# Kernel optimization log

Hardware: AMD Instinct MI355X
Metric: run time of the kernel (lower is better)

Reference implementation:

```python
import jax, jax.numpy as jnp
import numpy as np

N_NODES = 100000
N_EDGES = 1600000
N_GRAPHS = 256
EPS = 1e-5  # GraphNorm / BatchNorm eps


def _seg_sum(x, seg, n):
    return jax.ops.segment_sum(x, seg, num_segments=n)


def setup_inputs() -> dict:
    key = jax.random.key(0)
    ks = jax.random.split(key, 24)
    f32 = jnp.float32

    def nrm(k, shape, s=0.05):
        return jax.random.normal(k, shape, f32) * s

    inp = {}
    inp["x"] = jax.random.normal(ks[0], (N_NODES, 64), f32)
    inp["edge_attr"] = jax.random.normal(ks[1], (N_EDGES, 8), f32)
    # edge_mlp: Linear(8,16) -> ReLU -> Linear(16,1); final bias +2 keeps degrees positive
    inp["em_w1"] = nrm(ks[2], (16, 8), 0.1); inp["em_b1"] = jnp.zeros((16,), f32)
    inp["em_w2"] = nrm(ks[3], (1, 16), 0.1); inp["em_b2"] = jnp.full((1,), 2.0, f32)
    # GCNConv weights stored (in, out); PyG GCNConv lin has no bias, separate bias after aggregation
    inp["conv_w0"] = nrm(ks[4], (64, 128)); inp["conv_b0"] = jnp.zeros((128,), f32)
    inp["conv_w1"] = nrm(ks[5], (128, 128)); inp["conv_b1"] = jnp.zeros((128,), f32)
    inp["conv_w2"] = nrm(ks[6], (128, 128)); inp["conv_b2"] = jnp.zeros((128,), f32)
    # GraphNorm params: weight=1, bias=0, mean_scale=1 (PyG init)
    for i in range(3):
        inp[f"gn_w{i}"] = jnp.ones((128,), f32)
        inp[f"gn_b{i}"] = jnp.zeros((128,), f32)
        inp[f"gn_ms{i}"] = jnp.ones((128,), f32)
    # MLP head (weights stored (in,out)); BatchNorm1d eval: running_mean=0, running_var=1
    inp["lin_w0"] = nrm(ks[7], (128, 256)); inp["lin_b0"] = jnp.zeros((256,), f32)
    inp["bn_g0"] = jnp.ones((256,), f32); inp["bn_b0"] = jnp.zeros((256,), f32)
    inp["lin_w1"] = nrm(ks[8], (256, 128)); inp["lin_b1"] = jnp.zeros((128,), f32)
    inp["bn_g1"] = jnp.ones((128,), f32); inp["bn_b1"] = jnp.zeros((128,), f32)
    inp["out_w"] = nrm(ks[9], (128, 1)); inp["out_b"] = jnp.zeros((1,), f32)
    inp["edge_index"] = jax.random.randint(ks[10], (2, N_EDGES), 0, N_NODES)
    inp["batch"] = jnp.sort(jax.random.randint(ks[11], (N_NODES,), 0, N_GRAPHS))
    return inp


def _gcn_conv(h, W, b, src, tgt, ew):
    # PyG GCNConv with edge_weight: add self-loops (weight 1), symmetric normalization
    hw = h @ W  # [N, out]
    deg = _seg_sum(ew, tgt, N_NODES) + 1.0  # in-degree incl. self-loop
    dinv = jnp.where(deg > 0, jax.lax.rsqrt(deg), 0.0)
    norm_e = dinv[src] * ew * dinv[tgt]  # [E]
    agg = _seg_sum(norm_e[:, None] * hw[src], tgt, N_NODES)
    agg = agg + (dinv * dinv)[:, None] * hw  # self-loop contribution
    return agg + b


def _graph_norm(h, batch, w, b, ms, cnt):
    mean = _seg_sum(h, batch, N_GRAPHS) / cnt[:, None]  # [G, C]
    sub = h - ms * mean[batch]
    var = _seg_sum(sub * sub, batch, N_GRAPHS) / cnt[:, None]
    return w * sub / jnp.sqrt(var + EPS)[batch] + b


def reference(x, edge_attr, em_w1, em_b1, em_w2, em_b2,
              conv_w0, conv_b0, conv_w1, conv_b1, conv_w2, conv_b2,
              gn_w0, gn_b0, gn_ms0, gn_w1, gn_b1, gn_ms1, gn_w2, gn_b2, gn_ms2,
              lin_w0, lin_b0, bn_g0, bn_b0, lin_w1, lin_b1, bn_g1, bn_b1,
              out_w, out_b, edge_index, batch):
    src, tgt = edge_index[0], edge_index[1]
    ew = (jax.nn.relu(edge_attr @ em_w1.T + em_b1) @ em_w2.T + em_b2).reshape(-1)  # [E]
    cnt = jnp.maximum(_seg_sum(jnp.ones((N_NODES,), x.dtype), batch, N_GRAPHS), 1.0)

    h = x
    layers = [(conv_w0, conv_b0, gn_w0, gn_b0, gn_ms0),
              (conv_w1, conv_b1, gn_w1, gn_b1, gn_ms1),
              (conv_w2, conv_b2, gn_w2, gn_b2, gn_ms2)]
    for W, b, gw, gb, gms in layers:
        h = _gcn_conv(h, W, b, src, tgt, ew)
        h = _graph_norm(h, batch, gw, gb, gms, cnt)
        h = jax.nn.relu(h)  # dropout is identity in eval mode

    pooled = _seg_sum(h, batch, N_GRAPHS) / cnt[:, None]  # global_mean_pool [G, 128]

    inv = 1.0 / jnp.sqrt(1.0 + EPS)  # BatchNorm1d eval: mean=0, var=1
    h = jax.nn.relu((pooled @ lin_w0 + lin_b0) * inv * bn_g0 + bn_b0)
    h = jax.nn.relu((h @ lin_w1 + lin_b1) * inv * bn_g1 + bn_b1)
    out = h @ out_w + out_b  # [G, 1]
    return (out, h)
```

## Files before the change

kernel.cpp:

```cpp
#include <hip/hip_runtime.h>

#define N_NODES 100000
#define N_EDGES 1600000
#define N_GRAPHS 256
#define EPS 1e-5f

#define NBUCK 1024
#define NUSED 782
#define NBLK 256
#define EPB (N_EDGES / NBLK)

#define WB 128
#define W0B 32
#define SB 2
#define PREP_BLOCKS (WB + W0B + SB + NBLK)

typedef __attribute__((ext_vector_type(8))) short bfrag8;
typedef __attribute__((ext_vector_type(4))) float facc4;

__device__ __forceinline__ void fma4(float4& a, float s, const float4& w) {
  a.x += s * w.x; a.y += s * w.y; a.z += s * w.z; a.w += s * w.w;
}

__device__ __forceinline__ unsigned short f2bf(float f) {
  union { float f; unsigned u; } x;
  x.f = f;
  unsigned r = x.u + 0x7FFF + ((x.u >> 16) & 1);
  return (unsigned short)(r >> 16);
}
__device__ __forceinline__ unsigned packbf(float a, float b) {
  return (unsigned)f2bf(a) | ((unsigned)f2bf(b) << 16);
}
__device__ __forceinline__ float4 bf4(unsigned lo, unsigned hi) {
  union { unsigned u; float f; } a, b, c, d;
  a.u = lo << 16;
  b.u = lo & 0xFFFF0000u;
  c.u = hi << 16;
  d.u = hi & 0xFFFF0000u;
  return make_float4(a.f, b.f, c.f, d.f);
}
__device__ __forceinline__ float bfat(const unsigned* tb, int idx) {
  unsigned u = tb[idx >> 1];
  union { unsigned u; float f; } v;
  v.u = (idx & 1) ? (u & 0xFFFF0000u) : (u << 16);
  return v.f;
}

__global__ __launch_bounds__(256) void k_prep(
    const float* __restrict__ cw1, const float* __restrict__ cw2,
    unsigned short* __restrict__ wt1, unsigned short* __restrict__ wt2,
    const float* __restrict__ cw0, unsigned short* __restrict__ wt0,
    const int* __restrict__ batch, int* __restrict__ start,
    const int* __restrict__ tgt, int* __restrict__ hists,
    int* __restrict__ bcnt) {
  __shared__ int h[NBUCK];
  const int b = blockIdx.x;
  const int t = threadIdx.x;
  if (b < WB) {
    int half = b >> 6;
    int id = (b & 63) * 256 + t;
    const float* w = half ? cw2 : cw1;
    unsigned short* o = half ? wt2 : wt1;
    int n = id >> 7, k = id & 127;
    o[n * 128 + k] = f2bf(w[k * 128 + n]);
  } else if (b < WB + W0B) {
    int id = (b - WB) * 256 + t;
    if (id >= 8192) return;
    int n = id >> 6, k = id & 63;
    wt0[n * 64 + k] = f2bf(cw0[k * 128 + n]);
  } else if (b < WB + W0B + SB) {
    int g = (b - WB - W0B) * 256 + t;
    if (g > N_GRAPHS) return;
    int lo = 0, hi = N_NODES;
    while (lo < hi) {
      int mid = (lo + hi) >> 1;
      if (batch[mid] < g) lo = mid + 1; else hi = mid;
    }
    start[g] = lo;
  } else {
    const int blk = b - WB - W0B - SB;
    for (int i = t; i < NBUCK; i += 256) h[i] = 0;
    __syncthreads();
    const int s = blk * EPB, e = s + EPB;
    for (int j = s + t; j < e; j += 256) atomicAdd(&h[tgt[j] >> 7], 1);
    __syncthreads();
    for (int i = t; i < NBUCK; i += 256) {
      int v = h[i];
      hists[blk * NBUCK + i] = v;
      if (v) atomicAdd(&bcnt[i], v);
    }
  }
}

__global__ __launch_bounds__(1024) void k_bscan(const int* __restrict__ bcnt,
                                                int* __restrict__ bbase) {
  __shared__ int s[NBUCK];
  const int b = threadIdx.x;
  int v = bcnt[b];
  s[b] = v;
  __syncthreads();
  for (int off = 1; off < NBUCK; off <<= 1) {
    int u = (b >= off) ? s[b - off] : 0;
    __syncthreads();
    s[b] += u;
    __syncthreads();
  }
  bbase[b] = s[b] - v;
  if (b == NBUCK - 1) bbase[NBUCK] = N_EDGES;
}

__global__ __launch_bounds__(NBLK) void k_cursors(const int* __restrict__ hists,
                                                  const int* __restrict__ bbase,
                                                  int* __restrict__ cursor) {
  __shared__ int s[NBLK];
  const int b = blockIdx.x;
  const int k = threadIdx.x;
  int v = hists[k * NBUCK + b];
  s[k] = v;
  __syncthreads();
  for (int off = 1; off < NBLK; off <<= 1) {
    int u = (k >= off) ? s[k - off] : 0;
    __syncthreads();
    s[k] += u;
    __syncthreads();
  }
  cursor[b * NBLK + k] = bbase[b] + s[k] - v;
}

__global__ __launch_bounds__(256) void k_scatter(
    const float* __restrict__ ea, const float* __restrict__ w1,
    const float* __restrict__ b1, const float* __restrict__ w2,
    const float* __restrict__ b2, const int* __restrict__ src,
    const int* __restrict__ tgt, const int* __restrict__ cursor,
    uint2* __restrict__ mb) {
  __shared__ float W1[128], B1[16], W2[16];
  __shared__ int cur[NBUCK];
  const int blk = blockIdx.x, t = threadIdx.x;
  if (t < 128) W1[t] = w1[t];
  if (t < 16) { B1[t] = b1[t]; W2[t] = w2[t]; }
  for (int i = t; i < NUSED; i += 256) cur[i] = cursor[i * NBLK + blk];
  __syncthreads();
  const int s = blk * EPB, e = s + EPB;
  for (int j = s + t; j < e; j += 256) {
    const float4* ap = (const float4*)(ea + (size_t)j * 8);
    float4 a0 = ap[0], a1 = ap[1];
    float a[8] = {a0.x, a0.y, a0.z, a0.w, a1.x, a1.y, a1.z, a1.w};
    float out = b2[0];
#pragma unroll
    for (int i = 0; i < 16; ++i) {
      float h = B1[i];
#pragma unroll
      for (int jj = 0; jj < 8; ++jj) h += a[jj] * W1[i * 8 + jj];
      out += fmaxf(h, 0.f) * W2[i];
    }
    int d = tgt[j];
    int bin = d >> 7;
    int pos = atomicAdd(&cur[bin], 1);
    union { float f; unsigned u; } w;
    w.f = out;
    mb[pos] = make_uint2(w.u, (unsigned)src[j] | ((unsigned)(d & 127) << 25));
  }
}

__global__ __launch_bounds__(256) void k_csr(
    const uint2* __restrict__ mb, const int* __restrict__ bbase,
    const float* __restrict__ x, uint2* __restrict__ meta,
    int* __restrict__ rowstart, float* __restrict__ dinv,
    unsigned* __restrict__ xb) {
  __shared__ int hist[128];
  __shared__ float degf[128];
  __shared__ int cur[128];
  __shared__ float dls[128];
  const int b = blockIdx.x;
  const int t = threadIdx.x;
  const int s = bbase[b], e = bbase[b + 1];
  if (t < 128) { hist[t] = 0; degf[t] = 0.f; }
  __syncthreads();
  for (int j = s + t; j < e; j += 256) {
    uint2 m = mb[j];
    int bin = m.y >> 25;
    atomicAdd(&hist[bin], 1);
    union { unsigned u; float f; } w;
    w.u = m.x;
    atomicAdd(&degf[bin], w.f);
  }
  __syncthreads();
  int own = (t < 128) ? hist[t] : 0;
  for (int off = 1; off < 128; off <<= 1) {
    int u = (t >= off && t < 128) ? hist[t - off] : 0;
    __syncthreads();
    if (t < 128) hist[t] += u;
    __syncthreads();
  }
  if (t < 128) {
    int excl = hist[t] - own;
    int node = b * 128 + t;
    if (node <= N_NODES) rowstart[node] = s + excl;
    float dv = 0.f;
    if (node < N_NODES) {
      float d = 1.f + degf[t];
      dv = d > 0.f ? rsqrtf(d) : 0.f;
      dinv[node] = dv;
    }
    dls[t] = dv;
    cur[t] = s + excl;
  }
  __syncthreads();
  for (int j = s + t; j < e; j += 256) {
    uint2 m = mb[j];
    int bin = m.y >> 25;
    int pos = atomicAdd(&cur[bin], 1);
    meta[pos] = make_uint2(m.x, m.y & 0x1FFFFFFu);
  }
  {
    const int ln = t >> 1, half = t & 1;
    const int node = b * 128 + ln;
    if (node < N_NODES) {
      float dv = dls[ln];
      const float* px = x + (size_t)node * 64 + half * 32;
#pragma unroll
      for (int c8 = 0; c8 < 4; ++c8) {
        float4 a = *(const float4*)(px + c8 * 8);
        float4 bb = *(const float4*)(px + c8 * 8 + 4);
        uint4 o;
        o.x = packbf(dv * a.x, dv * a.y);
        o.y = packbf(dv * a.z, dv * a.w);
        o.z = packbf(dv * bb.x, dv * bb.y);
        o.w = packbf(dv * bb.z, dv * bb.w);
        *(uint4*)&xb[(size_t)node * 32 + half * 16 + c8 * 4] = o;
      }
    }
  }
}

__global__ __launch_bounds__(256) void k_gather64b(
    const unsigned* __restrict__ xb, const uint2* __restrict__ meta,
    const int* __restrict__ rowstart, const float* __restrict__ dinv,
    unsigned* __restrict__ aggxb) {
  const int t = threadIdx.x;
  const int n = blockIdx.x * 4 + (t >> 6);
  if (n >= N_NODES) return;
  const unsigned lane = t & 63;
  const unsigned q = lane >> 3;
  const unsigned cl = lane & 7;
  const int rs = rowstart[n], re = rowstart[n + 1];
  const uint4* x4 = (const uint4*)xb;
  float4 lo0 = make_float4(0.f, 0.f, 0.f, 0.f), hi0 = lo0;
  float4 lo1 = lo0, hi1 = lo0;
  int j = rs;
  for (; j + 16 <= re; j += 16) {
    uint2 m0 = meta[j + q], m1 = meta[j + 8 + q];
    union { unsigned u; float f; } w0, w1;
    w0.u = m0.x; w1.u = m1.x;
    uint4 v0 = x4[(m0.y << 3) + cl];
    uint4 v1 = x4[(m1.y << 3) + cl];
    fma4(lo0, w0.f, bf4(v0.x, v0.y));
    fma4(hi0, w0.f, bf4(v0.z, v0.w));
    fma4(lo1, w1.f, bf4(v1.x, v1.y));
    fma4(hi1, w1.f, bf4(v1.z, v1.w));
  }
  for (; j + 8 <= re; j += 8) {
    uint2 m0 = meta[j + q];
    union { unsigned u; float f; } w0;
    w0.u = m0.x;
    uint4 v0 = x4[(m0.y << 3) + cl];
    fma4(lo0, w0.f, bf4(v0.x, v0.y));
    fma4(hi0, w0.f, bf4(v0.z, v0.w));
  }
  if (j + (int)q < re) {
    uint2 m0 = meta[j + q];
    union { unsigned u; float f; } w0;
    w0.u = m0.x;
    uint4 v0 = x4[(m0.y << 3) + cl];
    fma4(lo1, w0.f, bf4(v0.x, v0.y));
    fma4(hi1, w0.f, bf4(v0.z, v0.w));
  }
  lo0.x += lo1.x; lo0.y += lo1.y; lo0.z += lo1.z; lo0.w += lo1.w;
  hi0.x += hi1.x; hi0.y += hi1.y; hi0.z += hi1.z; hi0.w += hi1.w;
#pragma unroll
  for (int m = 8; m <= 32; m <<= 1) {
    lo0.x += __shfl_xor(lo0.x, m);
    lo0.y += __shfl_xor(lo0.y, m);
    lo0.z += __shfl_xor(lo0.z, m);
    lo0.w += __shfl_xor(lo0.w, m);
    hi0.x += __shfl_xor(hi0.x, m);
    hi0.y += __shfl_xor(hi0.y, m);
    hi0.z += __shfl_xor(hi0.z, m);
    hi0.w += __shfl_xor(hi0.w, m);
  }
  if (q == 0) {
    float dv = dinv[n];
    uint4 sv = x4[((unsigned)n << 3) + cl];
    float4 slo = bf4(sv.x, sv.y), shi = bf4(sv.z, sv.w);
    uint4 o;
    o.x = packbf(dv * (lo0.x + slo.x), dv * (lo0.y + slo.y));
    o.y = packbf(dv * (lo0.z + slo.z), dv * (lo0.w + slo.w));
    o.z = packbf(dv * (hi0.x + shi.x), dv * (hi0.y + shi.y));
    o.w = packbf(dv * (hi0.z + shi.z), dv * (hi0.w + shi.w));
    ((uint4*)aggxb)[((unsigned)n << 3) + cl] = o;
  }
}

__global__ __launch_bounds__(256) void k_hw_mfma0(
    const unsigned short* __restrict__ aggxb,
    const unsigned short* __restrict__ wt0, const float* __restrict__ bias,
    unsigned short* __restrict__ h1b) {
  __shared__ unsigned short Asb[64][72];
  __shared__ unsigned short Wsb[128][72];
  const int t = threadIdx.x;
  const int base = blockIdx.x * 64;

  for (int i = t; i < 1024; i += 256) {
    int nr = i >> 3, k8 = (i & 7) * 8;
    *(uint4*)&Wsb[nr][k8] = *(const uint4*)&wt0[nr * 64 + k8];
  }
  {
    const int ln = t >> 2;
    const int kp = (t & 3) * 16;
    const int n = base + ln;
    if (n < N_NODES) {
      *(uint4*)&Asb[ln][kp] = *(const uint4*)&aggxb[(size_t)n * 64 + kp];
      *(uint4*)&Asb[ln][kp + 8] = *(const uint4*)&aggxb[(size_t)n * 64 + kp + 8];
    } else {
      uint4 z = make_uint4(0, 0, 0, 0);
      *(uint4*)&Asb[ln][kp] = z;
      *(uint4*)&Asb[ln][kp + 8] = z;
    }
  }
  __syncthreads();

  const int wv = t >> 6;
  const int lr = t & 15;
  const int lk = (t >> 4) & 3;
  const int m0 = wv * 16;

  bfrag8 af[2];
#pragma unroll
  for (int kc = 0; kc < 2; ++kc)
    af[kc] = *(const bfrag8*)&Asb[m0 + lr][kc * 32 + lk * 8];

#pragma unroll
  for (int nt = 0; nt < 8; ++nt) {
    facc4 c = {0.f, 0.f, 0.f, 0.f};
#pragma unroll
    for (int kc = 0; kc < 2; ++kc) {
      bfrag8 bf = *(const bfrag8*)&Wsb[nt * 16 + lr][kc * 32 + lk * 8];
      c = __builtin_amdgcn_mfma_f32_16x16x32_bf16(af[kc], bf, c, 0, 0, 0);
    }
    int col = nt * 16 + lr;
    float bv = bias[col];
#pragma unroll
    for (int r = 0; r < 4; ++r) {
      int n = base + m0 + lk * 4 + r;
      if (n < N_NODES) h1b[(size_t)n * 128 + col] = f2bf(c[r] + bv);
    }
  }
}

__global__ __launch_bounds__(256) void k_hw_mfma(
    const unsigned* __restrict__ hb, const unsigned short* __restrict__ wt,
    const int* __restrict__ batch, const float* __restrict__ An,
    const float* __restrict__ Bn, const float* __restrict__ dinv,
    unsigned short* __restrict__ hwb) {
  __shared__ unsigned short Asb[64][136];
  __shared__ unsigned short Wsb[128][136];
  const int t = threadIdx.x;
  const int base = blockIdx.x * 64;

  for (int i = t; i < 2048; i += 256) {
    int nr = i >> 4, k8 = (i & 15) * 8;
    *(uint4*)&Wsb[nr][k8] = *(const uint4*)&wt[nr * 128 + k8];
  }
  {
    const int ln = t >> 2;
    const int cg = (t & 3) * 32;
    const int n = base + ln;
    if (n < N_NODES) {
      const int g = batch[n];
      const uint4* hp = (const uint4*)(hb + (size_t)n * 64);
      const float* Ap = An + (size_t)g * 128;
      const float* Bp = Bn + (size_t)g * 128;
#pragma unroll
      for (int qq = 0; qq < 4; ++qq) {
        int c = cg + qq * 8;
        uint4 v = hp[(t & 3) * 4 + qq];
        float4 lo = bf4(v.x, v.y);
        float4 hi = bf4(v.z, v.w);
        float4 Alo = *(const float4*)&Ap[c], Blo = *(const float4*)&Bp[c];
        float4 Ahi = *(const float4*)&Ap[c + 4], Bhi = *(const float4*)&Bp[c + 4];
        uint4 o;
        o.x = packbf(fmaxf(Alo.x * lo.x + Blo.x, 0.f),
                     fmaxf(Alo.y * lo.y + Blo.y, 0.f));
        o.y = packbf(fmaxf(Alo.z * lo.z + Blo.z, 0.f),
                     fmaxf(Alo.w * lo.w + Blo.w, 0.f));
        o.z = packbf(fmaxf(Ahi.x * hi.x + Bhi.x, 0.f),
                     fmaxf(Ahi.y * hi.y + Bhi.y, 0.f));
        o.w = packbf(fmaxf(Ahi.z * hi.z + Bhi.z, 0.f),
                     fmaxf(Ahi.w * hi.w + Bhi.w, 0.f));
        *(uint4*)&Asb[ln][c] = o;
      }
    } else {
      uint4 z = make_uint4(0, 0, 0, 0);
#pragma unroll
      for (int qq = 0; qq < 4; ++qq) *(uint4*)&Asb[ln][cg + qq * 8] = z;
    }
  }
  __syncthreads();

  const int wv = t >> 6;
  const int lr = t & 15;
  const int lk = (t >> 4) & 3;
  const int m0 = wv * 16;

  bfrag8 af[4];
#pragma unroll
  for (int kc = 0; kc < 4; ++kc)
    af[kc] = *(const bfrag8*)&Asb[m0 + lr][kc * 32 + lk * 8];

  float dv[4];
#pragma unroll
  for (int r = 0; r < 4; ++r) {
    int n = base + m0 + lk * 4 + r;
    dv[r] = (n < N_NODES) ? dinv[n] : 0.f;
  }

#pragma unroll
  for (int nt = 0; nt < 8; ++nt) {
    facc4 c = {0.f, 0.f, 0.f, 0.f};
#pragma unroll
    for (int kc = 0; kc < 4; ++kc) {
      bfrag8 bf = *(const bfrag8*)&Wsb[nt * 16 + lr][kc * 32 + lk * 8];
      c = __builtin_amdgcn_mfma_f32_16x16x32_bf16(af[kc], bf, c, 0, 0, 0);
    }
    int col = nt * 16 + lr;
#pragma unroll
    for (int r = 0; r < 4; ++r) {
      int n = base + m0 + lk * 4 + r;
      if (n < N_NODES) hwb[(size_t)n * 128 + col] = f2bf(dv[r] * c[r]);
    }
  }
}

__global__ __launch_bounds__(256) void k_gatherb(
    const unsigned* __restrict__ hwb, const uint2* __restrict__ meta,
    const int* __restrict__ rowstart, const float* __restrict__ dinv,
    const float* __restrict__ bias, unsigned* __restrict__ aggb) {
  const int t = threadIdx.x;
  const int n = blockIdx.x * 4 + (t >> 6);
  if (n >= N_NODES) return;
  const unsigned lane = t & 63;
  const unsigned q = lane >> 4;
  const unsigned cl = lane & 15;
  const int rs = rowstart[n], re = rowstart[n + 1];
  const uint4* hb4 = (const uint4*)hwb;
  float4 lo0 = make_float4(0.f, 0.f, 0.f, 0.f), hi0 = lo0;
  float4 lo1 = lo0, hi1 = lo0;
  int j = rs;
  for (; j + 8 <= re; j += 8) {
    uint2 m0 = meta[j + q], m1 = meta[j + 4 + q];
    union { unsigned u; float f; } w0, w1;
    w0.u = m0.x; w1.u = m1.x;
    uint4 v0 = hb4[(m0.y << 4) + cl];
    uint4 v1 = hb4[(m1.y << 4) + cl];
    fma4(lo0, w0.f, bf4(v0.x, v0.y));
    fma4(hi0, w0.f, bf4(v0.z, v0.w));
    fma4(lo1, w1.f, bf4(v1.x, v1.y));
    fma4(hi1, w1.f, bf4(v1.z, v1.w));
  }
  for (; j + 4 <= re; j += 4) {
    uint2 m0 = meta[j + q];
    union { unsigned u; float f; } w0;
    w0.u = m0.x;
    uint4 v0 = hb4[(m0.y << 4) + cl];
    fma4(lo0, w0.f, bf4(v0.x, v0.y));
    fma4(hi0, w0.f, bf4(v0.z, v0.w));
  }
  if (j + (int)q < re) {
    uint2 m0 = meta[j + q];
    union { unsigned u; float f; } w0;
    w0.u = m0.x;
    uint4 v0 = hb4[(m0.y << 4) + cl];
    fma4(lo1, w0.f, bf4(v0.x, v0.y));
    fma4(hi1, w0.f, bf4(v0.z, v0.w));
  }
  lo0.x += lo1.x; lo0.y += lo1.y; lo0.z += lo1.z; lo0.w += lo1.w;
  hi0.x += hi1.x; hi0.y += hi1.y; hi0.z += hi1.z; hi0.w += hi1.w;
#pragma unroll
  for (int m = 16; m <= 32; m <<= 1) {
    lo0.x += __shfl_xor(lo0.x, m);
    lo0.y += __shfl_xor(lo0.y, m);
    lo0.z += __shfl_xor(lo0.z, m);
    lo0.w += __shfl_xor(lo0.w, m);
    hi0.x += __shfl_xor(hi0.x, m);
    hi0.y += __shfl_xor(hi0.y, m);
    hi0.z += __shfl_xor(hi0.z, m);
    hi0.w += __shfl_xor(hi0.w, m);
  }
  if (q == 0) {
    float dv = dinv[n];
    uint4 sv = hb4[((unsigned)n << 4) + cl];
    float4 slo = bf4(sv.x, sv.y), shi = bf4(sv.z, sv.w);
    float4 blo = *(const float4*)&bias[cl * 8];
    float4 bhi = *(const float4*)&bias[cl * 8 + 4];
    uint4 o;
    o.x = packbf(dv * (lo0.x + slo.x) + blo.x, dv * (lo0.y + slo.y) + blo.y);
    o.y = packbf(dv * (lo0.z + slo.z) + blo.z, dv * (lo0.w + slo.w) + blo.w);
    o.z = packbf(dv * (hi0.x + shi.x) + bhi.x, dv * (hi0.y + shi.y) + bhi.y);
    o.w = packbf(dv * (hi0.z + shi.z) + bhi.z, dv * (hi0.w + shi.w) + bhi.w);
    ((uint4*)aggb)[((unsigned)n << 4) + cl] = o;
  }
}

__global__ __launch_bounds__(512) void k_gstats(
    const unsigned* __restrict__ hb, const int* __restrict__ start,
    const float* __restrict__ gw, const float* __restrict__ gb,
    const float* __restrict__ gms, float* __restrict__ An,
    float* __restrict__ Bn) {
  int g = blockIdx.x;
  int s = start[g], e = start[g + 1];
  int t = threadIdx.x, p = t >> 7, c = t & 127;
  float sum = 0.f, sq = 0.f;
  for (int n = s + p; n < e; n += 4) {
    float v = bfat(hb + (size_t)n * 64, c);
    sum += v;
    sq += v * v;
  }
  __shared__ float S[4][128], Q[4][128];
  S[p][c] = sum;
  Q[p][c] = sq;
  __syncthreads();
  if (t < 128) {
    float cnt = (float)max(e - s, 1);
    float mean = (S[0][t] + S[1][t] + S[2][t] + S[3][t]) / cnt;
    float e2 = (Q[0][t] + Q[1][t] + Q[2][t] + Q[3][t]) / cnt;
    float ms = gms[t];
    float var = fmaxf(e2 - ms * (2.f - ms) * mean * mean, 0.f);
    float scale = gw[t] / sqrtf(var + EPS);
    An[(size_t)g * 128 + t] = scale;
    Bn[(size_t)g * 128 + t] = gb[t] - scale * ms * mean;
  }
}

__global__ __launch_bounds__(512) void k_gstats_pool(
    const unsigned* __restrict__ hb, const int* __restrict__ start,
    const float* __restrict__ gw, const float* __restrict__ gb,
    const float* __restrict__ gms, float* __restrict__ pooled) {
  int g = blockIdx.x;
  int s = start[g], e = start[g + 1];
  int t = threadIdx.x, p = t >> 7, c = t & 127;
  float sum = 0.f, sq = 0.f;
  for (int n = s + p; n < e; n += 4) {
    float v = bfat(hb + (size_t)n * 64, c);
    sum += v;
    sq += v * v;
  }
  __shared__ float S[4][128], Q[4][128], Af[128], Bf[128];
  S[p][c] = sum;
  Q[p][c] = sq;
  __syncthreads();
  if (t < 128) {
    float cnt = (float)max(e - s, 1);
    float mean = (S[0][t] + S[1][t] + S[2][t] + S[3][t]) / cnt;
    float e2 = (Q[0][t] + Q[1][t] + Q[2][t] + Q[3][t]) / cnt;
    float ms = gms[t];
    float var = fmaxf(e2 - ms * (2.f - ms) * mean * mean, 0.f);
    float scale = gw[t] / sqrtf(var + EPS);
    Af[t] = scale;
    Bf[t] = gb[t] - scale * ms * mean;
  }
  __syncthreads();
  float A = Af[c], B = Bf[c];
  float psum = 0.f;
  for (int n = s + p; n < e; n += 4)
    psum += fmaxf(A * bfat(hb + (size_t)n * 64, c) + B, 0.f);
  __syncthreads();
  S[p][c] = psum;
  __syncthreads();
  if (t < 128) {
    float cnt = (float)max(e - s, 1);
    pooled[g * 128 + t] = (S[0][t] + S[1][t] + S[2][t] + S[3][t]) / cnt;
  }
}

__global__ __launch_bounds__(256) void k_head(
    const float* __restrict__ pooled, const float* __restrict__ w0,
    const float* __restrict__ b0, const float* __restrict__ g0,
    const float* __restrict__ bb0, const float* __restrict__ w1,
    const float* __restrict__ b1, const float* __restrict__ g1,
    const float* __restrict__ bb1, const float* __restrict__ ow,
    const float* __restrict__ ob, float* __restrict__ out) {
  __shared__ float p[128], h1[256], h2[128];
  int g = blockIdx.x, t = threadIdx.x;
  const float inv = 1.0f / sqrtf(1.0f + EPS);
  if (t < 128) p[t] = pooled[g * 128 + t];
  __syncthreads();
  {
    float acc = b0[t];
#pragma unroll 8
    for (int k = 0; k < 128; ++k) acc += p[k] * w0[k * 256 + t];
    h1[t] = fmaxf(acc * inv * g0[t] + bb0[t], 0.f);
  }
  __syncthreads();
  if (t < 128) {
    float acc = b1[t];
#pragma unroll 8
    for (int k = 0; k < 256; ++k) acc += h1[k] * w1[k * 128 + t];
    float v = fmaxf(acc * inv * g1[t] + bb1[t], 0.f);
    h2[t] = v;
    out[N_GRAPHS + g * 128 + t] = v;
  }
  __syncthreads();
  if (t < 64) {
    float v = h2[t] * ow[t] + h2[t + 64] * ow[t + 64];
#pragma unroll
    for (int off = 32; off; off >>= 1) v += __shfl_down(v, off);
    if (t == 0) out[g] = v + ob[0];
  }
}

extern "C" void kernel_launch(void* const* d_in, const int* in_sizes, int n_in,
                              void* d_out, int out_size, void* d_ws,
                              size_t ws_size, hipStream_t stream) {
  const float* x = (const float*)d_in[0];
  const float* edge_attr = (const float*)d_in[1];
  const float* em_w1 = (const float*)d_in[2];
  const float* em_b1 = (const float*)d_in[3];
  const float* em_w2 = (const float*)d_in[4];
  const float* em_b2 = (const float*)d_in[5];
  const float* conv_w[3] = {(const float*)d_in[6], (const float*)d_in[8],
                            (const float*)d_in[10]};
  const float* conv_b[3] = {(const float*)d_in[7], (const float*)d_in[9],
                            (const float*)d_in[11]};
  const float* gn_w[3] = {(const float*)d_in[12], (const float*)d_in[15],
                          (const float*)d_in[18]};
  const float* gn_b[3] = {(const float*)d_in[13], (const float*)d_in[16],
                          (const float*)d_in[19]};
  const float* gn_ms[3] = {(const float*)d_in[14], (const float*)d_in[17],
                           (const float*)d_in[20]};
  const float* lin_w0 = (const float*)d_in[21];
  const float* lin_b0 = (const float*)d_in[22];
  const float* bn_g0 = (const float*)d_in[23];
  const float* bn_b0 = (const float*)d_in[24];
  const float* lin_w1 = (const float*)d_in[25];
  const float* lin_b1 = (const float*)d_in[26];
  const float* bn_g1 = (const float*)d_in[27];
  const float* bn_b1 = (const float*)d_in[28];
  const float* out_w = (const float*)d_in[29];
  const float* out_b = (const float*)d_in[30];
  const int* edge_index = (const int*)d_in[31];
  const int* batch = (const int*)d_in[32];
  const int* src = edge_index;
  const int* tgt = edge_index + N_EDGES;

  char* w = (char*)d_ws;
  size_t off = 0;
  auto carve = [&](size_t bytes) {
    void* p = w + off;
    off = (off + bytes + 511) & ~(size_t)511;
    return p;
  };
  float* dinv = (float*)carve((size_t)N_NODES * 4);
  int* rowstart = (int*)carve((size_t)(N_NODES + 1) * 4);
  int* hists = (int*)carve((size_t)NBLK * NBUCK * 4);
  int* cursor = (int*)carve((size_t)NBUCK * NBLK * 4);
  int* bcnt = (int*)carve((size_t)NBUCK * 4);
  int* bbase = (int*)carve((size_t)(NBUCK + 1) * 4);
  uint2* mb = (uint2*)carve((size_t)N_EDGES * 8);
  uint2* meta = (uint2*)carve((size_t)N_EDGES * 8);
  int* start = (int*)carve((N_GRAPHS + 1) * 4);
  float* AB = (float*)carve((size_t)4 * N_GRAPHS * 128 * 4);
  unsigned* xb = (unsigned*)carve((size_t)N_NODES * 64 * 2);
  unsigned* aggxb = (unsigned*)carve((size_t)N_NODES * 64 * 2);
  unsigned* h1b = (unsigned*)carve((size_t)N_NODES * 128 * 2);
  unsigned* hwb = (unsigned*)carve((size_t)N_NODES * 128 * 2);
  unsigned* agg1b = (unsigned*)carve((size_t)N_NODES * 128 * 2);
  unsigned* agg2b = (unsigned*)carve((size_t)N_NODES * 128 * 2);
  unsigned short* wt0 = (unsigned short*)carve((size_t)128 * 64 * 2);
  unsigned short* wt1 = (unsigned short*)carve((size_t)128 * 128 * 2);
  unsigned short* wt2 = (unsigned short*)carve((size_t)128 * 128 * 2);
  float* pooled = (float*)carve((size_t)N_GRAPHS * 128 * 4);

  float* A0 = AB, *B0 = AB + N_GRAPHS * 128;
  float* A1 = AB + 2 * N_GRAPHS * 128, *B1 = AB + 3 * N_GRAPHS * 128;

  hipMemsetAsync(bcnt, 0, (size_t)NBUCK * 4, stream);

  k_prep<<<PREP_BLOCKS, 256, 0, stream>>>(conv_w[1], conv_w[2], wt1, wt2,
                                          conv_w[0], wt0, batch, start, tgt,
                                          hists, bcnt);
  k_bscan<<<1, 1024, 0, stream>>>(bcnt, bbase);
  k_cursors<<<NUSED, NBLK, 0, stream>>>(hists, bbase, cursor);
  k_scatter<<<NBLK, 256, 0, stream>>>(edge_attr, em_w1, em_b1, em_w2, em_b2,
                                      src, tgt, cursor, mb);
  k_csr<<<NUSED, 256, 0, stream>>>(mb, bbase, x, meta, rowstart, dinv, xb);

  const int ggrid = (N_NODES + 3) / 4;
  const int hwgrid = (N_NODES + 63) / 64;

  k_gather64b<<<ggrid, 256, 0, stream>>>(xb, meta, rowstart, dinv, aggxb);
  k_hw_mfma0<<<hwgrid, 256, 0, stream>>>((unsigned short*)aggxb, wt0,
                                         conv_b[0], (unsigned short*)h1b);
  k_gstats<<<N_GRAPHS, 512, 0, stream>>>(h1b, start, gn_w[0], gn_b[0],
                                         gn_ms[0], A0, B0);
  k_hw_mfma<<<hwgrid, 256, 0, stream>>>(h1b, wt1, batch, A0, B0, dinv,
                                        (unsigned short*)hwb);
  k_gatherb<<<ggrid, 256, 0, stream>>>(hwb, meta, rowstart, dinv, conv_b[1],
                                       agg1b);
  k_gstats<<<N_GRAPHS, 512, 0, stream>>>(agg1b, start, gn_w[1], gn_b[1],
                                         gn_ms[1], A1, B1);
  k_hw_mfma<<<hwgrid, 256, 0, stream>>>(agg1b, wt2, batch, A1, B1, dinv,
                                        (unsigned short*)hwb);
  k_gatherb<<<ggrid, 256, 0, stream>>>(hwb, meta, rowstart, dinv, conv_b[2],
                                       agg2b);
  k_gstats_pool<<<N_GRAPHS, 512, 0, stream>>>(agg2b, start, gn_w[2], gn_b[2],
                                              gn_ms[2], pooled);

  k_head<<<N_GRAPHS, 256, 0, stream>>>(pooled, lin_w0, lin_b0, bn_g0, bn_b0,
                                       lin_w1, lin_b1, bn_g1, bn_b1, out_w,
                                       out_b, (float*)d_out);
}
```

Before: 489.4 us.

## Fuse layer-0 neighbor gather into the MFMA GEMM kernel via shared memory

New measurement: 488.6 us. About the same (-0.2%).

```diff
diff --git a/kernel.cpp b/kernel.cpp
--- a/kernel.cpp
+++ b/kernel.cpp
@@ -233,76 +233,9 @@
   }
 }
 
-__global__ __launch_bounds__(256) void k_gather64b(
+__global__ __launch_bounds__(256) void k_l0(
     const unsigned* __restrict__ xb, const uint2* __restrict__ meta,
     const int* __restrict__ rowstart, const float* __restrict__ dinv,
-    unsigned* __restrict__ aggxb) {
-  const int t = threadIdx.x;
-  const int n = blockIdx.x * 4 + (t >> 6);
-  if (n >= N_NODES) return;
-  const unsigned lane = t & 63;
-  const unsigned q = lane >> 3;
-  const unsigned cl = lane & 7;
-  const int rs = rowstart[n], re = rowstart[n + 1];
-  const uint4* x4 = (const uint4*)xb;
-  float4 lo0 = make_float4(0.f, 0.f, 0.f, 0.f), hi0 = lo0;
-  float4 lo1 = lo0, hi1 = lo0;
-  int j = rs;
-  for (; j + 16 <= re; j += 16) {
-    uint2 m0 = meta[j + q], m1 = meta[j + 8 + q];
-    union { unsigned u; float f; } w0, w1;
-    w0.u = m0.x; w1.u = m1.x;
-    uint4 v0 = x4[(m0.y << 3) + cl];
-    uint4 v1 = x4[(m1.y << 3) + cl];
-    fma4(lo0, w0.f, bf4(v0.x, v0.y));
-    fma4(hi0, w0.f, bf4(v0.z, v0.w));
-    fma4(lo1, w1.f, bf4(v1.x, v1.y));
-    fma4(hi1, w1.f, bf4(v1.z, v1.w));
-  }
-  for (; j + 8 <= re; j += 8) {
-    uint2 m0 = meta[j + q];
-    union { unsigned u; float f; } w0;
-    w0.u = m0.x;
-    uint4 v0 = x4[(m0.y << 3) + cl];
-    fma4(lo0, w0.f, bf4(v0.x, v0.y));
-    fma4(hi0, w0.f, bf4(v0.z, v0.w));
-  }
-  if (j + (int)q < re) {
-    uint2 m0 = meta[j + q];
-    union { unsigned u; float f; } w0;
-    w0.u = m0.x;
-    uint4 v0 = x4[(m0.y << 3) + cl];
-    fma4(lo1, w0.f, bf4(v0.x, v0.y));
-    fma4(hi1, w0.f, bf4(v0.z, v0.w));
-  }
-  lo0.x += lo1.x; lo0.y += lo1.y; lo0.z += lo1.z; lo0.w += lo1.w;
-  hi0.x += hi1.x; hi0.y += hi1.y; hi0.z += hi1.z; hi0.w += hi1.w;
-#pragma unroll
-  for (int m = 8; m <= 32; m <<= 1) {
-    lo0.x += __shfl_xor(lo0.x, m);
-    lo0.y += __shfl_xor(lo0.y, m);
-    lo0.z += __shfl_xor(lo0.z, m);
-    lo0.w += __shfl_xor(lo0.w, m);
-    hi0.x += __shfl_xor(hi0.x, m);
-    hi0.y += __shfl_xor(hi0.y, m);
-    hi0.z += __shfl_xor(hi0.z, m);
-    hi0.w += __shfl_xor(hi0.w, m);
-  }
-  if (q == 0) {
-    float dv = dinv[n];
-    uint4 sv = x4[((unsigned)n << 3) + cl];
-    float4 slo = bf4(sv.x, sv.y), shi = bf4(sv.z, sv.w);
-    uint4 o;
-    o.x = packbf(dv * (lo0.x + slo.x), dv * (lo0.y + slo.y));
-    o.y = packbf(dv * (lo0.z + slo.z), dv * (lo0.w + slo.w));
-    o.z = packbf(dv * (hi0.x + shi.x), dv * (hi0.y + shi.y));
-    o.w = packbf(dv * (hi0.z + shi.z), dv * (hi0.w + shi.w));
-    ((uint4*)aggxb)[((unsigned)n << 3) + cl] = o;
-  }
-}
-
-__global__ __launch_bounds__(256) void k_hw_mfma0(
-    const unsigned short* __restrict__ aggxb,
     const unsigned short* __restrict__ wt0, const float* __restrict__ bias,
     unsigned short* __restrict__ h1b) {
   __shared__ unsigned short Asb[64][72];
@@ -314,22 +247,81 @@
     int nr = i >> 3, k8 = (i & 7) * 8;
     *(uint4*)&Wsb[nr][k8] = *(const uint4*)&wt0[nr * 64 + k8];
   }
-  {
-    const int ln = t >> 2;
-    const int kp = (t & 3) * 16;
+
+  const int wv = t >> 6;
+  const unsigned lane = t & 63;
+  const unsigned q = lane >> 3;
+  const unsigned cl = lane & 7;
+  const uint4* x4 = (const uint4*)xb;
+
+  for (int it = 0; it < 16; ++it) {
+    const int ln = wv * 16 + it;
     const int n = base + ln;
-    if (n < N_NODES) {
-      *(uint4*)&Asb[ln][kp] = *(const uint4*)&aggxb[(size_t)n * 64 + kp];
-      *(uint4*)&Asb[ln][kp + 8] = *(const uint4*)&aggxb[(size_t)n * 64 + kp + 8];
-    } else {
-      uint4 z = make_uint4(0, 0, 0, 0);
-      *(uint4*)&Asb[ln][kp] = z;
-      *(uint4*)&Asb[ln][kp + 8] = z;
-    }
-  }
-  __syncthreads();
-
-  const int wv = t >> 6;
+    if (n >= N_NODES) {
+      if (q == 0) {
+        uint4 z = make_uint4(0, 0, 0, 0);
+        *(uint4*)&Asb[ln][cl * 8] = z;
+      }
+      continue;
+    }
+    const int rs = rowstart[n], re = rowstart[n + 1];
+    float4 lo0 = make_float4(0.f, 0.f, 0.f, 0.f), hi0 = lo0;
+    float4 lo1 = lo0, hi1 = lo0;
+    int j = rs;
+    for (; j + 16 <= re; j += 16) {
+      uint2 m0 = meta[j + q], m1 = meta[j + 8 + q];
+      union { unsigned u; float f; } w0, w1;
+      w0.u = m0.x; w1.u = m1.x;
+      uint4 v0 = x4[(m0.y << 3) + cl];
+      uint4 v1 = x4[(m1.y << 3) + cl];
+      fma4(lo0, w0.f, bf4(v0.x, v0.y));
+      fma4(hi0, w0.f, bf4(v0.z, v0.w));
+      fma4(lo1, w1.f, bf4(v1.x, v1.y));
+      fma4(hi1, w1.f, bf4(v1.z, v1.w));
+    }
+    for (; j + 8 <= re; j += 8) {
+      uint2 m0 = meta[j + q];
+      union { unsigned u; float f; } w0;
+      w0.u = m0.x;
+      uint4 v0 = x4[(m0.y << 3) + cl];
+      fma4(lo0, w0.f, bf4(v0.x, v0.y));
+      fma4(hi0, w0.f, bf4(v0.z, v0.w));
+    }
+    if (j + (int)q < re) {
+      uint2 m0 = meta[j + q];
+      union { unsigned u; float f; } w0;
+      w0.u = m0.x;
+      uint4 v0 = x4[(m0.y << 3) + cl];
+      fma4(lo1, w0.f, bf4(v0.x, v0.y));
+      fma4(hi1, w0.f, bf4(v0.z, v0.w));
+    }
+    lo0.x += lo1.x; lo0.y += lo1.y; lo0.z += lo1.z; lo0.w += lo1.w;
+    hi0.x += hi1.x; hi0.y += hi1.y; hi0.z += hi1.z; hi0.w += hi1.w;
+#pragma unroll
+    for (int m = 8; m <= 32; m <<= 1) {
+      lo0.x += __shfl_xor(lo0.x, m);
+      lo0.y += __shfl_xor(lo0.y, m);
+      lo0.z += __shfl_xor(lo0.z, m);
+      lo0.w += __shfl_xor(lo0.w, m);
+      hi0.x += __shfl_xor(hi0.x, m);
+      hi0.y += __shfl_xor(hi0.y, m);
+      hi0.z += __shfl_xor(hi0.z, m);
+      hi0.w += __shfl_xor(hi0.w, m);
+    }
+    if (q == 0) {
+      float dv = dinv[n];
+      uint4 sv = x4[((unsigned)n << 3) + cl];
+      float4 slo = bf4(sv.x, sv.y), shi = bf4(sv.z, sv.w);
+      uint4 o;
+      o.x = packbf(dv * (lo0.x + slo.x), dv * (lo0.y + slo.y));
+      o.y = packbf(dv * (lo0.z + slo.z), dv * (lo0.w + slo.w));
+      o.z = packbf(dv * (hi0.x + shi.x), dv * (hi0.y + shi.y));
+      o.w = packbf(dv * (hi0.z + shi.z), dv * (hi0.w + shi.w));
+      *(uint4*)&Asb[ln][cl * 8] = o;
+    }
+  }
+  __syncthreads();
+
   const int lr = t & 15;
   const int lk = (t >> 4) & 3;
   const int m0 = wv * 16;
@@ -670,7 +662,6 @@
   int* start = (int*)carve((N_GRAPHS + 1) * 4);
   float* AB = (float*)carve((size_t)4 * N_GRAPHS * 128 * 4);
   unsigned* xb = (unsigned*)carve((size_t)N_NODES * 64 * 2);
-  unsigned* aggxb = (unsigned*)carve((size_t)N_NODES * 64 * 2);
   unsigned* h1b = (unsigned*)carve((size_t)N_NODES * 128 * 2);
   unsigned* hwb = (unsigned*)carve((size_t)N_NODES * 128 * 2);
   unsigned* agg1b = (unsigned*)carve((size_t)N_NODES * 128 * 2);
@@ -697,9 +688,8 @@
   const int ggrid = (N_NODES + 3) / 4;
   const int hwgrid = (N_NODES + 63) / 64;
 
-  k_gather64b<<<ggrid, 256, 0, stream>>>(xb, meta, rowstart, dinv, aggxb);
-  k_hw_mfma0<<<hwgrid, 256, 0, stream>>>((unsigned short*)aggxb, wt0,
-                                         conv_b[0], (unsigned short*)h1b);
+  k_l0<<<hwgrid, 256, 0, stream>>>(xb, meta, rowstart, dinv, wt0, conv_b[0],
+                                   (unsigned short*)h1b);
   k_gstats<<<N_GRAPHS, 512, 0, stream>>>(h1b, start, gn_w[0], gn_b[0],
                                          gn_ms[0], A0, B0);
   k_hw_mfma<<<hwgrid, 256, 0, stream>>>(h1b, wt1, batch, A0, B0, dinv,
```
